# Kernel tuning notes

Hardware: AMD Instinct MI355X
Metric: run time of the kernel (lower is better)

The kernel has to match this reference:

```python
import jax, jax.numpy as jnp
import numpy as np

HIDDEN = 512
LATENT = 256
NUM_NODE_TYPES = 16


def setup_inputs() -> dict:
    key = jax.random.key(0)
    ks = jax.random.split(key, 9)
    s = lambda fan_in: 1.0 / np.sqrt(fan_in)
    return {
        "z": jax.random.normal(ks[0], (1024, LATENT), dtype=jnp.float32),
        "num_nodes": 128,
        "W_z": jax.random.uniform(ks[1], (LATENT, HIDDEN), jnp.float32, -s(LATENT), s(LATENT)),
        "b_z": jax.random.uniform(ks[2], (HIDDEN,), jnp.float32, -s(LATENT), s(LATENT)),
        "W_node": jax.random.uniform(ks[3], (HIDDEN, NUM_NODE_TYPES), jnp.float32, -s(HIDDEN), s(HIDDEN)),
        "b_node": jax.random.uniform(ks[4], (NUM_NODE_TYPES,), jnp.float32, -s(HIDDEN), s(HIDDEN)),
        "W_e1": jax.random.uniform(ks[5], (2 * HIDDEN, HIDDEN), jnp.float32, -s(2 * HIDDEN), s(2 * HIDDEN)),
        "b_e1": jax.random.uniform(ks[6], (HIDDEN,), jnp.float32, -s(2 * HIDDEN), s(2 * HIDDEN)),
        "W_e2": jax.random.uniform(ks[7], (HIDDEN, 1), jnp.float32, -s(HIDDEN), s(HIDDEN)),
        "b_e2": jax.random.uniform(ks[8], (1,), jnp.float32, -s(HIDDEN), s(HIDDEN)),
    }


def reference(z, num_nodes, W_z, b_z, W_node, b_node, W_e1, b_e1, W_e2, b_e2):
    # h: [B, H]
    h = jax.nn.relu(z @ W_z + b_z)
    B = z.shape[0]
    # h_expanded: [B, N, H] (same h replicated per node, as in the original)
    h_expanded = jnp.broadcast_to(h[:, None, :], (B, num_nodes, h.shape[-1]))
    node_logits = h_expanded @ W_node + b_node  # [B, N, T]
    # Every (i, j) pair in the original loop uses cat(h, h) -> identical scalar per batch.
    h_pair = jnp.concatenate([h, h], axis=-1)  # [B, 2H]
    p = jax.nn.sigmoid(jax.nn.relu(h_pair @ W_e1 + b_e1) @ W_e2 + b_e2)  # [B, 1]
    # Scatter onto strict lower triangle (j < i), zeros elsewhere.
    tril = jnp.tril(jnp.ones((num_nodes, num_nodes), dtype=z.dtype), k=-1)  # [N, N]
    edge_probs = p[:, :, None] * tril[None, :, :]  # [B, N, N]
    return node_logits, edge_probs
```

## Files before the change

kernel.cpp:

```cpp
#include <hip/hip_runtime.h>
#include <hip/hip_bf16.h>

#define BB 1024
#define LL 256
#define HH 512
#define TT 16
#define NN 128

#define NODE_F4 (BB * NN * TT / 4)
#define EDGE_F4 (BB * NN * NN / 4)

typedef short bf16x8 __attribute__((ext_vector_type(8)));
typedef float f32x4  __attribute__((ext_vector_type(4)));

__global__ __launch_bounds__(256) void k_conv(const float* __restrict__ in,
                                              __hip_bfloat16* __restrict__ out) {
    const int q = blockIdx.x * 256 + threadIdx.x;
    float4 v = ((const float4*)in)[q];
    out[4 * q + 0] = __float2bfloat16(v.x);
    out[4 * q + 1] = __float2bfloat16(v.y);
    out[4 * q + 2] = __float2bfloat16(v.z);
    out[4 * q + 3] = __float2bfloat16(v.w);
}

template <bool FOLD>
__global__ __launch_bounds__(256) void k_transconv(const float* __restrict__ in,
                                                   __hip_bfloat16* __restrict__ out,
                                                   int Kdim, int Ndim) {
    __shared__ __hip_bfloat16 tile[32][33];
    const int tx = threadIdx.x & 31;
    const int ty = threadIdx.x >> 5;
    const int k0 = blockIdx.y * 32;
    const int n0 = blockIdx.x * 32;
    #pragma unroll
    for (int r = ty; r < 32; r += 8) {
        float v = in[(k0 + r) * Ndim + n0 + tx];
        if (FOLD) v += in[(k0 + r + HH) * Ndim + n0 + tx];
        tile[r][tx] = __float2bfloat16(v);
    }
    __syncthreads();
    #pragma unroll
    for (int r = ty; r < 32; r += 8) {
        out[(n0 + r) * Kdim + k0 + tx] = tile[tx][r];
    }
}

template <int K>
__global__ __launch_bounds__(256) void k_mfma_gemm(const __hip_bfloat16* __restrict__ A,
                                                   const __hip_bfloat16* __restrict__ Bt,
                                                   const float* __restrict__ bias,
                                                   __hip_bfloat16* __restrict__ out) {
    const int wid  = (blockIdx.x << 2) + (threadIdx.x >> 6);
    const int lane = threadIdx.x & 63;
    const int mt   = wid >> 5;
    const int nt   = wid & 31;
    const int l16  = lane & 15;
    const int quad = lane >> 4;

    const short* Ap = (const short*)A  + (mt * 16 + l16) * K + quad * 8;
    const short* Bp = (const short*)Bt + (nt * 16 + l16) * K + quad * 8;

    f32x4 acc = {0.f, 0.f, 0.f, 0.f};
    #pragma unroll
    for (int kt = 0; kt < K / 32; ++kt) {
        bf16x8 a = *(const bf16x8*)(Ap + kt * 32);
        bf16x8 b = *(const bf16x8*)(Bp + kt * 32);
        acc = __builtin_amdgcn_mfma_f32_16x16x32_bf16(a, b, acc, 0, 0, 0);
    }

    const float bb = bias[nt * 16 + l16];
    #pragma unroll
    for (int r = 0; r < 4; ++r) {
        float v = fmaxf(acc[r] + bb, 0.f);
        out[(mt * 16 + quad * 4 + r) * HH + nt * 16 + l16] = __float2bfloat16(v);
    }
}

__global__ __launch_bounds__(256) void k_head(const __hip_bfloat16* __restrict__ h,
                                              const __hip_bfloat16* __restrict__ e1,
                                              const float* __restrict__ Wn,
                                              const float* __restrict__ bn,
                                              const float* __restrict__ We2,
                                              const float* __restrict__ be2,
                                              float* __restrict__ node16,
                                              float* __restrict__ p) {
    const int b   = blockIdx.x;
    const int tid = threadIdx.x;
    __shared__ float hs[HH];
    __shared__ float red[256];

    hs[tid]       = __bfloat162float(h[b * HH + tid]);
    hs[tid + 256] = __bfloat162float(h[b * HH + tid + 256]);
    __syncthreads();

    const int o = tid & 15, part = tid >> 4;
    float s = 0.f;
    #pragma unroll 4
    for (int kk = 0; kk < 32; ++kk) {
        const int k = part * 32 + kk;
        s += hs[k] * Wn[k * TT + o];
    }
    red[tid] = s;
    __syncthreads();
    if (tid < 16) {
        float t = 0.f;
        #pragma unroll
        for (int q = 0; q < 16; ++q) t += red[q * 16 + tid];
        node16[b * TT + tid] = t + bn[tid];
    }
    __syncthreads();

    float s2 = __bfloat162float(e1[b * HH + tid]) * We2[tid]
             + __bfloat162float(e1[b * HH + tid + 256]) * We2[tid + 256];
    #pragma unroll
    for (int off = 32; off; off >>= 1) s2 += __shfl_down(s2, off);
    if ((tid & 63) == 0) red[tid >> 6] = s2;
    __syncthreads();
    if (tid == 0) {
        float t = red[0] + red[1] + red[2] + red[3] + be2[0];
        p[b] = 1.f / (1.f + __expf(-t));
    }
}

__global__ __launch_bounds__(256) void k_write(const float* __restrict__ node16,
                                               const float* __restrict__ p,
                                               float4* __restrict__ out) {
    const int q = blockIdx.x * 256 + threadIdx.x;
    if (q < NODE_F4) {
        const int b  = q >> 9;
        const int t4 = q & 3;
        out[q] = ((const float4*)(node16 + b * TT))[t4];
    } else {
        const int e  = q - NODE_F4;
        const int b  = e >> 12;
        const int i  = (e >> 5) & 127;
        const int j0 = (e & 31) * 4;
        const float pv = p[b];
        float4 v;
        v.x = (j0 + 0 < i) ? pv : 0.f;
        v.y = (j0 + 1 < i) ? pv : 0.f;
        v.z = (j0 + 2 < i) ? pv : 0.f;
        v.w = (j0 + 3 < i) ? pv : 0.f;
        out[q] = v;
    }
}

extern "C" void kernel_launch(void* const* d_in, const int* in_sizes, int n_in,
                              void* d_out, int out_size, void* d_ws, size_t ws_size,
                              hipStream_t stream) {
    const float* z    = (const float*)d_in[0];
    const float* Wz   = (const float*)d_in[2];
    const float* bz   = (const float*)d_in[3];
    const float* Wn   = (const float*)d_in[4];
    const float* bn   = (const float*)d_in[5];
    const float* We1  = (const float*)d_in[6];
    const float* be1  = (const float*)d_in[7];
    const float* We2  = (const float*)d_in[8];
    const float* be2  = (const float*)d_in[9];
    float* out = (float*)d_out;

    char* base = (char*)d_ws;
    __hip_bfloat16* z_bf  = (__hip_bfloat16*)(base);
    __hip_bfloat16* WzT   = (__hip_bfloat16*)(base +  512 * 1024);
    __hip_bfloat16* WsumT = (__hip_bfloat16*)(base +  768 * 1024);
    __hip_bfloat16* h_bf  = (__hip_bfloat16*)(base + 1280 * 1024);
    __hip_bfloat16* e1_bf = (__hip_bfloat16*)(base + 2304 * 1024);
    float*          node16 = (float*)(base + 3328 * 1024);
    float*          p      = (float*)(base + 3392 * 1024);

    k_conv<<<BB * LL / 4 / 256, 256, 0, stream>>>(z, z_bf);

    k_transconv<false><<<dim3(HH / 32, LL / 32), 256, 0, stream>>>(Wz, WzT, LL, HH);

    k_transconv<true><<<dim3(HH / 32, HH / 32), 256, 0, stream>>>(We1, WsumT, HH, HH);

    k_mfma_gemm<LL><<<512, 256, 0, stream>>>(z_bf, WzT, bz, h_bf);

    k_mfma_gemm<HH><<<512, 256, 0, stream>>>(h_bf, WsumT, be1, e1_bf);

    k_head<<<BB, 256, 0, stream>>>(h_bf, e1_bf, Wn, bn, We2, be2, node16, p);

    k_write<<<(NODE_F4 + EDGE_F4) / 256, 256, 0, stream>>>(node16, p, (float4*)out);

    (void)in_sizes; (void)n_in; (void)out_size; (void)ws_size;
}
```

Before: 130.9 us.

## Merge prep kernels, fuse edge head into GEMM2 epilogue, use MFMA for node head

Merges the z conversion and both weight transposes into one prep kernel that also transposes W_node and zeroes an accumulator. The second GEMM now applies ReLU, multiplies by W_e2 and reduces across columns with shuffles and atomics, so the e1 intermediate is never written. The node logits head runs as a small MFMA GEMM. The aim is fewer launches and less intermediate traffic, at the cost of atomic contention and non-deterministic summation order.

Result: faster. 127.4 us (-2.7%).

```diff
diff --git a/kernel.cpp b/kernel.cpp
--- a/kernel.cpp
+++ b/kernel.cpp
@@ -1,5 +1,6 @@
 #include <hip/hip_runtime.h>
 #include <hip/hip_bf16.h>
+#include <math.h>
 
 #define BB 1024
 #define LL 256
@@ -11,31 +12,24 @@
 #define EDGE_F4 (BB * NN * NN / 4)
 
 typedef short bf16x8 __attribute__((ext_vector_type(8)));
+typedef short s16x4  __attribute__((ext_vector_type(4)));
 typedef float f32x4  __attribute__((ext_vector_type(4)));
 
-__global__ __launch_bounds__(256) void k_conv(const float* __restrict__ in,
-                                              __hip_bfloat16* __restrict__ out) {
-    const int q = blockIdx.x * 256 + threadIdx.x;
-    float4 v = ((const float4*)in)[q];
-    out[4 * q + 0] = __float2bfloat16(v.x);
-    out[4 * q + 1] = __float2bfloat16(v.y);
-    out[4 * q + 2] = __float2bfloat16(v.z);
-    out[4 * q + 3] = __float2bfloat16(v.w);
-}
-
-template <bool FOLD>
-__global__ __launch_bounds__(256) void k_transconv(const float* __restrict__ in,
-                                                   __hip_bfloat16* __restrict__ out,
-                                                   int Kdim, int Ndim) {
-    __shared__ __hip_bfloat16 tile[32][33];
+static __device__ __forceinline__ short bfbits(float f) {
+    __hip_bfloat16 h = __float2bfloat16(f);
+    return *reinterpret_cast<short*>(&h);
+}
+
+__device__ __forceinline__ void transpose_tile(const float* __restrict__ in,
+                                               __hip_bfloat16* __restrict__ out,
+                                               int k0, int n0, int Kdim, bool fold,
+                                               __hip_bfloat16 (*tile)[34]) {
     const int tx = threadIdx.x & 31;
     const int ty = threadIdx.x >> 5;
-    const int k0 = blockIdx.y * 32;
-    const int n0 = blockIdx.x * 32;
     #pragma unroll
     for (int r = ty; r < 32; r += 8) {
-        float v = in[(k0 + r) * Ndim + n0 + tx];
-        if (FOLD) v += in[(k0 + r + HH) * Ndim + n0 + tx];
+        float v = in[(k0 + r) * HH + n0 + tx];
+        if (fold) v += in[(k0 + r + HH) * HH + n0 + tx];
         tile[r][tx] = __float2bfloat16(v);
     }
     __syncthreads();
@@ -45,80 +39,133 @@
     }
 }
 
-template <int K>
-__global__ __launch_bounds__(256) void k_mfma_gemm(const __hip_bfloat16* __restrict__ A,
-                                                   const __hip_bfloat16* __restrict__ Bt,
-                                                   const float* __restrict__ bias,
-                                                   __hip_bfloat16* __restrict__ out) {
+__global__ __launch_bounds__(256) void k_prep(const float* __restrict__ z,
+                                              const float* __restrict__ Wz,
+                                              const float* __restrict__ We1,
+                                              const float* __restrict__ Wn,
+                                              __hip_bfloat16* __restrict__ z_bf,
+                                              __hip_bfloat16* __restrict__ WzT,
+                                              __hip_bfloat16* __restrict__ WsumT,
+                                              __hip_bfloat16* __restrict__ WnT,
+                                              float* __restrict__ p_acc) {
+    __shared__ __hip_bfloat16 tile[32][34];
+    const int bid = blockIdx.x;
+    const int tid = threadIdx.x;
+    if (bid < 256) {
+        const int q = bid * 256 + tid;
+        float4 v = ((const float4*)z)[q];
+        s16x4 o; o.x = bfbits(v.x); o.y = bfbits(v.y); o.z = bfbits(v.z); o.w = bfbits(v.w);
+        ((s16x4*)z_bf)[q] = o;
+    } else if (bid < 384) {
+        const int t = bid - 256;
+        transpose_tile(Wz, WzT, (t >> 4) * 32, (t & 15) * 32, LL, false, tile);
+    } else if (bid < 640) {
+        const int t = bid - 384;
+        transpose_tile(We1, WsumT, (t >> 4) * 32, (t & 15) * 32, HH, true, tile);
+    } else if (bid < 672) {
+        const int u = (bid - 640) * 256 + tid;
+        const int tt = u >> 9, k = u & 511;
+        WnT[u] = __float2bfloat16(Wn[k * TT + tt]);
+    } else {
+        ((float4*)p_acc)[tid] = make_float4(0.f, 0.f, 0.f, 0.f);
+    }
+}
+
+__global__ __launch_bounds__(256) void k_gemm1(const __hip_bfloat16* __restrict__ A,
+                                               const __hip_bfloat16* __restrict__ Bt,
+                                               const float* __restrict__ bias,
+                                               __hip_bfloat16* __restrict__ out) {
     const int wid  = (blockIdx.x << 2) + (threadIdx.x >> 6);
     const int lane = threadIdx.x & 63;
-    const int mt   = wid >> 5;
-    const int nt   = wid & 31;
-    const int l16  = lane & 15;
-    const int quad = lane >> 4;
-
-    const short* Ap = (const short*)A  + (mt * 16 + l16) * K + quad * 8;
-    const short* Bp = (const short*)Bt + (nt * 16 + l16) * K + quad * 8;
+    const int mt = wid >> 5, nt = wid & 31;
+    const int l16 = lane & 15, quad = lane >> 4;
+
+    const short* Ap = (const short*)A  + (mt * 16 + l16) * LL + quad * 8;
+    const short* Bp = (const short*)Bt + (nt * 16 + l16) * LL + quad * 8;
 
     f32x4 acc = {0.f, 0.f, 0.f, 0.f};
     #pragma unroll
-    for (int kt = 0; kt < K / 32; ++kt) {
+    for (int kt = 0; kt < LL / 32; ++kt) {
         bf16x8 a = *(const bf16x8*)(Ap + kt * 32);
         bf16x8 b = *(const bf16x8*)(Bp + kt * 32);
         acc = __builtin_amdgcn_mfma_f32_16x16x32_bf16(a, b, acc, 0, 0, 0);
     }
-
-    const float bb = bias[nt * 16 + l16];
+    const int col = nt * 16 + l16;
+    const float bb = bias[col];
     #pragma unroll
     for (int r = 0; r < 4; ++r) {
-        float v = fmaxf(acc[r] + bb, 0.f);
-        out[(mt * 16 + quad * 4 + r) * HH + nt * 16 + l16] = __float2bfloat16(v);
-    }
-}
-
-__global__ __launch_bounds__(256) void k_head(const __hip_bfloat16* __restrict__ h,
-                                              const __hip_bfloat16* __restrict__ e1,
-                                              const float* __restrict__ Wn,
-                                              const float* __restrict__ bn,
-                                              const float* __restrict__ We2,
-                                              const float* __restrict__ be2,
-                                              float* __restrict__ node16,
-                                              float* __restrict__ p) {
-    const int b   = blockIdx.x;
-    const int tid = threadIdx.x;
-    __shared__ float hs[HH];
-    __shared__ float red[256];
-
-    hs[tid]       = __bfloat162float(h[b * HH + tid]);
-    hs[tid + 256] = __bfloat162float(h[b * HH + tid + 256]);
-    __syncthreads();
-
-    const int o = tid & 15, part = tid >> 4;
-    float s = 0.f;
-    #pragma unroll 4
-    for (int kk = 0; kk < 32; ++kk) {
-        const int k = part * 32 + kk;
-        s += hs[k] * Wn[k * TT + o];
-    }
-    red[tid] = s;
-    __syncthreads();
-    if (tid < 16) {
-        float t = 0.f;
+        out[(mt * 16 + quad * 4 + r) * HH + col] = __float2bfloat16(fmaxf(acc[r] + bb, 0.f));
+    }
+}
+
+__global__ __launch_bounds__(256) void k_gemm2_phead(const __hip_bfloat16* __restrict__ A,
+                                                     const __hip_bfloat16* __restrict__ Bt,
+                                                     const float* __restrict__ be1,
+                                                     const float* __restrict__ We2,
+                                                     float* __restrict__ p_acc) {
+    const int wid  = (blockIdx.x << 2) + (threadIdx.x >> 6);
+    const int lane = threadIdx.x & 63;
+    const int mt = wid >> 5, nt = wid & 31;
+    const int l16 = lane & 15, quad = lane >> 4;
+
+    const short* Ap = (const short*)A  + (mt * 16 + l16) * HH + quad * 8;
+    const short* Bp = (const short*)Bt + (nt * 16 + l16) * HH + quad * 8;
+
+    f32x4 acc = {0.f, 0.f, 0.f, 0.f};
+    #pragma unroll
+    for (int kt = 0; kt < HH / 32; ++kt) {
+        bf16x8 a = *(const bf16x8*)(Ap + kt * 32);
+        bf16x8 b = *(const bf16x8*)(Bp + kt * 32);
+        acc = __builtin_amdgcn_mfma_f32_16x16x32_bf16(a, b, acc, 0, 0, 0);
+    }
+    const int col = nt * 16 + l16;
+    const float bb = be1[col];
+    const float w2 = We2[col];
+    float sr[4];
+    #pragma unroll
+    for (int r = 0; r < 4; ++r) sr[r] = fmaxf(acc[r] + bb, 0.f) * w2;
+    #pragma unroll
+    for (int off = 1; off < 16; off <<= 1) {
         #pragma unroll
-        for (int q = 0; q < 16; ++q) t += red[q * 16 + tid];
-        node16[b * TT + tid] = t + bn[tid];
-    }
-    __syncthreads();
-
-    float s2 = __bfloat162float(e1[b * HH + tid]) * We2[tid]
-             + __bfloat162float(e1[b * HH + tid + 256]) * We2[tid + 256];
-    #pragma unroll
-    for (int off = 32; off; off >>= 1) s2 += __shfl_down(s2, off);
-    if ((tid & 63) == 0) red[tid >> 6] = s2;
-    __syncthreads();
-    if (tid == 0) {
-        float t = red[0] + red[1] + red[2] + red[3] + be2[0];
-        p[b] = 1.f / (1.f + __expf(-t));
+        for (int r = 0; r < 4; ++r) sr[r] += __shfl_xor(sr[r], off);
+    }
+    if (l16 == 0) {
+        #pragma unroll
+        for (int r = 0; r < 4; ++r)
+            atomicAdd(p_acc + mt * 16 + quad * 4 + r, sr[r]);
+    }
+}
+
+__global__ __launch_bounds__(256) void k_small(const __hip_bfloat16* __restrict__ h,
+                                               const __hip_bfloat16* __restrict__ WnT,
+                                               const float* __restrict__ bn,
+                                               const float* __restrict__ p_acc,
+                                               const float* __restrict__ be2,
+                                               float* __restrict__ node16,
+                                               float* __restrict__ p) {
+    const int wid  = (blockIdx.x << 2) + (threadIdx.x >> 6);
+    const int lane = threadIdx.x & 63;
+    const int l16 = lane & 15, quad = lane >> 4;
+
+    const short* Ap = (const short*)h   + (wid * 16 + l16) * HH + quad * 8;
+    const short* Bp = (const short*)WnT + l16 * HH + quad * 8;
+
+    f32x4 acc = {0.f, 0.f, 0.f, 0.f};
+    #pragma unroll
+    for (int kt = 0; kt < HH / 32; ++kt) {
+        bf16x8 a = *(const bf16x8*)(Ap + kt * 32);
+        bf16x8 b = *(const bf16x8*)(Bp + kt * 32);
+        acc = __builtin_amdgcn_mfma_f32_16x16x32_bf16(a, b, acc, 0, 0, 0);
+    }
+    const float bb = bn[l16];
+    #pragma unroll
+    for (int r = 0; r < 4; ++r)
+        node16[(wid * 16 + quad * 4 + r) * TT + l16] = acc[r] + bb;
+
+    const int idx = blockIdx.x * 256 + threadIdx.x;
+    if (idx < BB) {
+        float t = p_acc[idx] + be2[0];
+        p[idx] = 1.f / (1.f + expf(-t));
     }
 }
 
@@ -160,25 +207,22 @@
     float* out = (float*)d_out;
 
     char* base = (char*)d_ws;
-    __hip_bfloat16* z_bf  = (__hip_bfloat16*)(base);
-    __hip_bfloat16* WzT   = (__hip_bfloat16*)(base +  512 * 1024);
-    __hip_bfloat16* WsumT = (__hip_bfloat16*)(base +  768 * 1024);
-    __hip_bfloat16* h_bf  = (__hip_bfloat16*)(base + 1280 * 1024);
-    __hip_bfloat16* e1_bf = (__hip_bfloat16*)(base + 2304 * 1024);
-    float*          node16 = (float*)(base + 3328 * 1024);
-    float*          p      = (float*)(base + 3392 * 1024);
-
-    k_conv<<<BB * LL / 4 / 256, 256, 0, stream>>>(z, z_bf);
-
-    k_transconv<false><<<dim3(HH / 32, LL / 32), 256, 0, stream>>>(Wz, WzT, LL, HH);
-
-    k_transconv<true><<<dim3(HH / 32, HH / 32), 256, 0, stream>>>(We1, WsumT, HH, HH);
-
-    k_mfma_gemm<LL><<<512, 256, 0, stream>>>(z_bf, WzT, bz, h_bf);
-
-    k_mfma_gemm<HH><<<512, 256, 0, stream>>>(h_bf, WsumT, be1, e1_bf);
-
-    k_head<<<BB, 256, 0, stream>>>(h_bf, e1_bf, Wn, bn, We2, be2, node16, p);
+    __hip_bfloat16* z_bf   = (__hip_bfloat16*)(base);
+    __hip_bfloat16* WzT    = (__hip_bfloat16*)(base +  512 * 1024);
+    __hip_bfloat16* WsumT  = (__hip_bfloat16*)(base +  768 * 1024);
+    __hip_bfloat16* WnT    = (__hip_bfloat16*)(base + 1280 * 1024);
+    __hip_bfloat16* h_bf   = (__hip_bfloat16*)(base + 1296 * 1024);
+    float*          node16 = (float*)(base + 2320 * 1024);
+    float*          p_acc  = (float*)(base + 2384 * 1024);
+    float*          p      = (float*)(base + 2388 * 1024);
+
+    k_prep<<<673, 256, 0, stream>>>(z, Wz, We1, Wn, z_bf, WzT, WsumT, WnT, p_acc);
+
+    k_gemm1<<<512, 256, 0, stream>>>(z_bf, WzT, bz, h_bf);
+
+    k_gemm2_phead<<<512, 256, 0, stream>>>(h_bf, WsumT, be1, We2, p_acc);
+
+    k_small<<<16, 256, 0, stream>>>(h_bf, WnT, bn, p_acc, be2, node16, p);
 
     k_write<<<(NODE_F4 + EDGE_F4) / 256, 256, 0, stream>>>(node16, p, (float4*)out);
 
```
